# Kernel optimization log

Hardware: AMD Instinct MI355X
Metric: run time of the kernel (lower is better)

## Reference

```python
import jax, jax.numpy as jnp
import numpy as np
import math

FACTOR = 1

def setup_inputs() -> dict:
    key = jax.random.key(0)
    kq, kk, kv = jax.random.split(key, 3)
    B, L, H, D = 8, 4096, 8, 32
    queries = jax.random.normal(kq, (B, L, H, D), dtype=jnp.float32)
    keys = jax.random.normal(kk, (B, L, H, D), dtype=jnp.float32)
    values = jax.random.normal(kv, (B, L, H, D), dtype=jnp.float32)
    return {"queries": queries, "keys": keys, "values": values}


def reference(queries, keys, values):
    # queries/keys/values: [B, L, H, D]
    B, L, H, D = queries.shape
    q = jnp.transpose(queries, (0, 2, 1, 3))  # [B,H,L,D]
    k = jnp.transpose(keys, (0, 2, 1, 3))
    v = jnp.transpose(values, (0, 2, 1, 3))

    # FFT-based cross-correlation (period-based dependency discovery)
    q_fft = jnp.fft.rfft(q, axis=2)
    k_fft = jnp.fft.rfft(k, axis=2)
    spd = jnp.sum(q_fft * jnp.conj(k_fft), axis=-1)      # [B,H,Lf]
    corr = jnp.fft.irfft(spd, n=L, axis=-1)              # [B,H,L]

    # Time-delay aggregation (inference path: per-sample delays)
    top_k = max(1, min(int(FACTOR * math.log(L)), L))
    weights, delays = jax.lax.top_k(corr, top_k)          # [B,H,K]
    weights = jax.nn.softmax(weights, axis=-1)

    # roll values by -delay via circular gather: pattern[l] = v[(l+delay) % L]
    init_index = jnp.arange(L)[None, None, None, :]       # [1,1,1,L]
    idx = (init_index + delays[..., None]) % L            # [B,H,K,L]
    patterns = jnp.take_along_axis(v[:, :, None, :, :], idx[..., None], axis=3)  # [B,H,K,L,D]
    agg = jnp.sum(patterns * weights[..., None, None], axis=2)  # [B,H,L,D]

    # dropout is identity in eval mode
    return jnp.transpose(agg, (0, 2, 1, 3))  # [B,L,H,D]
```

## Files before the change

kernel.cpp:

```cpp
#include <hip/hip_runtime.h>
#include <hip/hip_bf16.h>


#define SWZ(i) ((i) ^ (((i) >> 4) & 15))
#define SLICE 2056

typedef float nfloat4 __attribute__((ext_vector_type(4)));

__device__ inline void cmul(float& outr, float& outi, float ar, float ai, float br, float bi) {
    outr = ar * br - ai * bi;
    outi = ar * bi + ai * br;
}

template<int DIR>
__device__ inline void fft16(float* vr, float* vi) {
    const float C1 = 0.92387953251128675613f;
    const float S1 = 0.38268343236508977173f;
    const float R2 = 0.70710678118654752440f;
    float ur[16], ui[16];
#pragma unroll
    for (int n2 = 0; n2 < 4; ++n2) {
        float ar = vr[n2],      ai = vi[n2];
        float br = vr[n2 + 4],  bi = vi[n2 + 4];
        float cr = vr[n2 + 8],  ci = vi[n2 + 8];
        float dr = vr[n2 + 12], di = vi[n2 + 12];
        float acr = ar + cr, aci = ai + ci;
        float asr = ar - cr, asi = ai - ci;
        float bdr = br + dr, bdi = bi + di;
        float bsr = br - dr, bsi = bi - di;
        ur[0 + n2]  = acr + bdr; ui[0 + n2]  = aci + bdi;
        ur[8 + n2]  = acr - bdr; ui[8 + n2]  = aci - bdi;
        if (DIR < 0) {
            ur[4 + n2]  = asr + bsi; ui[4 + n2]  = asi - bsr;
            ur[12 + n2] = asr - bsi; ui[12 + n2] = asi + bsr;
        } else {
            ur[4 + n2]  = asr - bsi; ui[4 + n2]  = asi + bsr;
            ur[12 + n2] = asr + bsi; ui[12 + n2] = asi - bsr;
        }
    }
#pragma unroll
    for (int k1 = 1; k1 < 4; ++k1) {
#pragma unroll
        for (int n2 = 1; n2 < 4; ++n2) {
            int e = k1 * n2;
            float c, s;
            if (e == 1)      { c = C1;  s = S1; }
            else if (e == 2) { c = R2;  s = R2; }
            else if (e == 3) { c = S1;  s = C1; }
            else if (e == 4) { c = 0.f; s = 1.f; }
            else if (e == 6) { c = -R2; s = R2; }
            else             { c = -C1; s = -S1; }
            int idx = k1 * 4 + n2;
            float r0 = ur[idx], i0 = ui[idx];
            if (DIR < 0) { ur[idx] = r0 * c + i0 * s; ui[idx] = i0 * c - r0 * s; }
            else         { ur[idx] = r0 * c - i0 * s; ui[idx] = i0 * c + r0 * s; }
        }
    }
#pragma unroll
    for (int k1 = 0; k1 < 4; ++k1) {
        float ar = ur[k1 * 4 + 0], ai = ui[k1 * 4 + 0];
        float br = ur[k1 * 4 + 1], bi = ui[k1 * 4 + 1];
        float cr = ur[k1 * 4 + 2], ci = ui[k1 * 4 + 2];
        float dr = ur[k1 * 4 + 3], di = ui[k1 * 4 + 3];
        float acr = ar + cr, aci = ai + ci;
        float asr = ar - cr, asi = ai - ci;
        float bdr = br + dr, bdi = bi + di;
        float bsr = br - dr, bsi = bi - di;
        vr[k1]      = acr + bdr; vi[k1]      = aci + bdi;
        vr[k1 + 8]  = acr - bdr; vi[k1 + 8]  = aci - bdi;
        if (DIR < 0) {
            vr[k1 + 4]  = asr + bsi; vi[k1 + 4]  = asi - bsr;
            vr[k1 + 12] = asr - bsi; vi[k1 + 12] = asi + bsr;
        } else {
            vr[k1 + 4]  = asr - bsi; vi[k1 + 4]  = asi + bsr;
            vr[k1 + 12] = asr + bsi; vi[k1 + 12] = asi - bsr;
        }
    }
}

template<int DIR, int NS>
__device__ inline void fft_pass16_pp(const float2* __restrict__ src,
                                     float2* __restrict__ dst,
                                     float w1r, float w1i, int j) {
    float vr[16], vi[16];
#pragma unroll
    for (int r = 0; r < 16; ++r) {
        float2 x = src[SWZ(j + r * 256)];
        vr[r] = x.x; vi[r] = x.y;
    }
    if (NS > 1) {
        float wr[16], wi[16];
        wr[1] = w1r; wi[1] = w1i;
#pragma unroll
        for (int r = 2; r < 16; ++r)
            cmul(wr[r], wi[r], wr[r >> 1], wi[r >> 1], wr[(r + 1) >> 1], wi[(r + 1) >> 1]);
#pragma unroll
        for (int r = 1; r < 16; ++r) {
            float r0 = vr[r], i0 = vi[r];
            vr[r] = r0 * wr[r] - i0 * wi[r];
            vi[r] = r0 * wi[r] + i0 * wr[r];
        }
    }
    fft16<DIR>(vr, vi);
    int base = (j / NS) * (16 * NS) + (j & (NS - 1));
#pragma unroll
    for (int r = 0; r < 16; ++r)
        dst[SWZ(base + r * NS)] = make_float2(vr[r], vi[r]);
}

template<int DIR>
__device__ inline void fft4096_pp(float2* A, float2* Bu, float c2, float s2,
                                  float c3, float s3, int tid) {
    fft_pass16_pp<DIR, 1>(A, Bu, 1.f, 0.f, tid);  __syncthreads();
    fft_pass16_pp<DIR, 16>(Bu, A, c2, s2, tid);   __syncthreads();
    fft_pass16_pp<DIR, 256>(A, Bu, c3, s3, tid);  __syncthreads();
}

__global__ __launch_bounds__(256) void transpose_pack_kernel(const float4* __restrict__ q4,
                                                             const float4* __restrict__ k4,
                                                             float4* __restrict__ xT4) {
    __shared__ float qs[64][65];
    __shared__ float ks[64][65];
    int bid = blockIdx.x;
    int ct = bid & 3;
    int lt = (bid >> 2) & 63;
    int b  = bid >> 8;
    int tid = threadIdx.x;
    int l0 = lt * 64, c0 = ct * 64;
    int cw = tid & 15;
    int rr = tid >> 4;
#pragma unroll
    for (int it = 0; it < 4; ++it) {
        int row = it * 16 + rr;
        size_t g = (size_t)(b * 4096 + l0 + row) * 64u + (size_t)(c0 / 4 + cw);
        float4 qv = q4[g];
        float4 kv = k4[g];
        qs[row][cw * 4 + 0] = qv.x; qs[row][cw * 4 + 1] = qv.y;
        qs[row][cw * 4 + 2] = qv.z; qs[row][cw * 4 + 3] = qv.w;
        ks[row][cw * 4 + 0] = kv.x; ks[row][cw * 4 + 1] = kv.y;
        ks[row][cw * 4 + 2] = kv.z; ks[row][cw * 4 + 3] = kv.w;
    }
    __syncthreads();
    int a = tid & 31;
    int cb = tid >> 5;
#pragma unroll
    for (int it = 0; it < 8; ++it) {
        int cc = it * 8 + cb;
        float4 o;
        o.x = qs[2 * a][cc];     o.y = ks[2 * a][cc];
        o.z = qs[2 * a + 1][cc]; o.w = ks[2 * a + 1][cc];
        xT4[(size_t)(b * 256 + c0 + cc) * 2048u + (size_t)(l0 / 2 + a)] = o;
    }
}

__device__ inline void spd_pair_accum(const float2* Z, float4* acc, float& accny, int tid) {
#pragma unroll
    for (int t = 0; t < 4; ++t) {
        int f0 = 2 * tid + 512 * t;
        float2 za = Z[SWZ(f0)];
        float2 zb = Z[SWZ(f0 + 1)];
        float2 ma = Z[SWZ((4096 - f0) & 4095)];
        float2 mb = Z[SWZ(4095 - f0)];
        float qr = za.x + ma.x, qi = za.y - ma.y;
        float kr = za.y + ma.y, ki = za.x - ma.x;
        acc[t].x += 0.25f * (qr * kr - qi * ki);
        acc[t].y += 0.25f * (qr * ki + qi * kr);
        qr = zb.x + mb.x; qi = zb.y - mb.y;
        kr = zb.y + mb.y; ki = zb.x - mb.x;
        acc[t].z += 0.25f * (qr * kr - qi * ki);
        acc[t].w += 0.25f * (qr * ki + qi * kr);
    }
    float2 zn = Z[SWZ(2048)];
    accny += zn.x * zn.y;
}

__global__ __launch_bounds__(256) void fwd_spd_fast(const float2* __restrict__ xT,
                                                    float2* __restrict__ spd_d) {
    __shared__ float2 A[4096], Bu[4096];
    int bid = blockIdx.x;
    int tid = threadIdx.x;
    int b = bid >> 6, p = bid & 63;
    const float TWO_PI = 6.2831853071795864769f;
    float ang2 = TWO_PI * (float)((tid & 15) * 16) * (1.0f / 4096.0f);
    float ang3 = TWO_PI * (float)tid * (1.0f / 4096.0f);
    float c2 = cosf(ang2), s2 = sinf(ang2);
    float c3 = cosf(ang3), s3 = sinf(ang3);
    float4 acc[4];
#pragma unroll
    for (int t = 0; t < 4; ++t) acc[t] = make_float4(0.f, 0.f, 0.f, 0.f);
    float accny = 0.f;
#pragma unroll
    for (int cc = 0; cc < 4; ++cc) {
        const float4* src4 = (const float4*)(xT + (size_t)(b * 256 + p * 4 + cc) * 4096u);
#pragma unroll
        for (int t = 0; t < 8; ++t) {
            float4 x = src4[tid + t * 256];
            int n = 2 * (tid + t * 256);
            A[SWZ(n)]     = make_float2(x.x, x.y);
            A[SWZ(n + 1)] = make_float2(x.z, x.w);
        }
        __syncthreads();
        fft4096_pp<-1>(A, Bu, c2, -s2, c3, -s3, tid);
        spd_pair_accum(Bu, acc, accny, tid);
        if (cc < 3) __syncthreads();
    }
    float4* dst4 = (float4*)(spd_d + (size_t)bid * SLICE);
#pragma unroll
    for (int t = 0; t < 4; ++t) dst4[tid + t * 256] = acc[t];
    if (tid == 0) spd_d[(size_t)bid * SLICE + 2048] = make_float2(accny, 0.f);
}

__global__ __launch_bounds__(256) void fwd_spd_slow(const float* __restrict__ q,
                                                    const float* __restrict__ k,
                                                    float2* __restrict__ spd_d) {
    __shared__ float2 A[4096], Bu[4096];
    int bid = blockIdx.x;
    int tid = threadIdx.x;
    int b = bid >> 6, p = bid & 63;
    const float TWO_PI = 6.2831853071795864769f;
    float ang2 = TWO_PI * (float)((tid & 15) * 16) * (1.0f / 4096.0f);
    float ang3 = TWO_PI * (float)tid * (1.0f / 4096.0f);
    float c2 = cosf(ang2), s2 = sinf(ang2);
    float c3 = cosf(ang3), s3 = sinf(ang3);
    float4 acc[4];
#pragma unroll
    for (int t = 0; t < 4; ++t) acc[t] = make_float4(0.f, 0.f, 0.f, 0.f);
    float accny = 0.f;
#pragma unroll
    for (int cc = 0; cc < 4; ++cc) {
        size_t base = (size_t)b * 1048576u + (size_t)(p * 4 + cc);
#pragma unroll
        for (int t = 0; t < 16; ++t) {
            int n = tid + t * 256;
            A[SWZ(n)] = make_float2(q[base + (size_t)n * 256u], k[base + (size_t)n * 256u]);
        }
        __syncthreads();
        fft4096_pp<-1>(A, Bu, c2, -s2, c3, -s3, tid);
        spd_pair_accum(Bu, acc, accny, tid);
        if (cc < 3) __syncthreads();
    }
    float4* dst4 = (float4*)(spd_d + (size_t)bid * SLICE);
#pragma unroll
    for (int t = 0; t < 4; ++t) dst4[tid + t * 256] = acc[t];
    if (tid == 0) spd_d[(size_t)bid * SLICE + 2048] = make_float2(accny, 0.f);
}

__global__ __launch_bounds__(256) void ifft_topk_kernel(const float2* __restrict__ spd_d,
                                                        float* __restrict__ wout,
                                                        int* __restrict__ dout) {
    __shared__ float2 A[4096], Bu[4096];
    __shared__ float rv[8][4];
    __shared__ int   ri[8][4];
    int bh = blockIdx.x;
    int b = bh >> 3, h = bh & 7;
    int tid = threadIdx.x;
    const float TWO_PI = 6.2831853071795864769f;
    float ang2 = TWO_PI * (float)((tid & 15) * 16) * (1.0f / 4096.0f);
    float ang3 = TWO_PI * (float)tid * (1.0f / 4096.0f);
    float c2 = cosf(ang2), s2 = sinf(ang2);
    float c3 = cosf(ang3), s3 = sinf(ang3);
    const float sc = 1.0f / 4096.0f;
    const float2* base = spd_d + (size_t)(b * 64 + h * 8) * SLICE;
    const float4* base4 = (const float4*)base;
#pragma unroll
    for (int t = 0; t < 4; ++t) {
        int f0 = 2 * tid + 512 * t;
        float4 a = make_float4(0.f, 0.f, 0.f, 0.f);
#pragma unroll
        for (int s = 0; s < 8; ++s) {
            float4 x = base4[(size_t)s * (SLICE / 2) + (size_t)(tid + 256 * t)];
            a.x += x.x; a.y += x.y; a.z += x.z; a.w += x.w;
        }
        float r0 = a.x * sc, i0 = a.y * sc;
        float r1 = a.z * sc, i1 = a.w * sc;
        A[SWZ(f0)]     = make_float2(r0, i0);
        A[SWZ(f0 + 1)] = make_float2(r1, i1);
        if (f0 > 0) A[SWZ(4096 - f0)] = make_float2(r0, -i0);
        A[SWZ(4095 - f0)] = make_float2(r1, -i1);
    }
    if (tid == 0) {
        float ny = 0.f;
#pragma unroll
        for (int s = 0; s < 8; ++s) ny += base[(size_t)s * SLICE + 2048].x;
        A[SWZ(2048)] = make_float2(ny * sc, 0.f);
    }
    __syncthreads();
    fft4096_pp<1>(A, Bu, c2, s2, c3, s3, tid);
    float cv[16];
#pragma unroll
    for (int t = 0; t < 16; ++t) cv[t] = Bu[SWZ(tid + t * 256)].x;

    int lane = tid & 63, wid = tid >> 6;
    float topv[8]; int topi[8];
    for (int kk = 0; kk < 8; ++kk) {
        float best = -3.0e38f; int bi = 0;
#pragma unroll
        for (int t = 0; t < 16; ++t) {
            int f = tid + t * 256;
            if (cv[t] > best) { best = cv[t]; bi = f; }
        }
#pragma unroll
        for (int off = 32; off > 0; off >>= 1) {
            float ov = __shfl_xor(best, off, 64);
            int   oi = __shfl_xor(bi, off, 64);
            if (ov > best || (ov == best && oi < bi)) { best = ov; bi = oi; }
        }
        if (lane == 0) { rv[kk][wid] = best; ri[kk][wid] = bi; }
        __syncthreads();
        float fb = rv[kk][0]; int fi = ri[kk][0];
#pragma unroll
        for (int w = 1; w < 4; ++w) {
            float ov = rv[kk][w]; int oi = ri[kk][w];
            if (ov > fb || (ov == fb && oi < fi)) { fb = ov; fi = oi; }
        }
        topv[kk] = fb; topi[kk] = fi;
        if (tid == (fi & 255)) {
            int t_owner = fi >> 8;
#pragma unroll
            for (int t = 0; t < 16; ++t)
                if (t == t_owner) cv[t] = -3.0e38f;
        }
    }
    if (tid == 0) {
        float mx = topv[0];
        float e[8], s = 0.0f;
#pragma unroll
        for (int kk = 0; kk < 8; ++kk) { e[kk] = expf(topv[kk] - mx); s += e[kk]; }
        float inv = 1.0f / s;
#pragma unroll
        for (int kk = 0; kk < 8; ++kk) {
            wout[bh * 8 + kk] = e[kk] * inv;
            dout[bh * 8 + kk] = topi[kk];
        }
    }
}

__global__ __launch_bounds__(256) void agg_kernel(const float4* __restrict__ v4,
                                                  const float* __restrict__ w,
                                                  const int* __restrict__ dl,
                                                  float4* __restrict__ out4) {
    __shared__ float sw[64];
    __shared__ int   sd[64];
    int blk = blockIdx.x;
    int b = blk & 7, lg = blk >> 3;
    int tid = threadIdx.x;
    if (tid < 64) {
        int h = tid >> 3, kk = tid & 7;
        sw[tid] = w[(b * 8 + h) * 8 + kk];
        sd[tid] = dl[(b * 8 + h) * 8 + kk];
    }
    __syncthreads();
    int lq = tid >> 6;
    int c4 = tid & 63;
    int h  = c4 >> 3;
    float w_[8]; int d_[8];
#pragma unroll
    for (int kk = 0; kk < 8; ++kk) { w_[kk] = sw[h * 8 + kk]; d_[kk] = sd[h * 8 + kk]; }
#pragma unroll
    for (int rep = 0; rep < 8; ++rep) {
        int l = lg * 32 + rep * 4 + lq;
        float4 acc = make_float4(0.f, 0.f, 0.f, 0.f);
#pragma unroll
        for (int kk = 0; kk < 8; ++kk) {
            int l2 = (l + d_[kk]) & 4095;
            float4 x = v4[(size_t)(b * 4096 + l2) * 64u + (size_t)c4];
            acc.x += w_[kk] * x.x; acc.y += w_[kk] * x.y;
            acc.z += w_[kk] * x.z; acc.w += w_[kk] * x.w;
        }
        nfloat4 nv = {acc.x, acc.y, acc.z, acc.w};
        __builtin_nontemporal_store(nv,
            (nfloat4*)&out4[(size_t)(b * 4096 + l) * 64u + (size_t)c4]);
    }
}

extern "C" void kernel_launch(void* const* d_in, const int* in_sizes, int n_in,
                              void* d_out, int out_size, void* d_ws, size_t ws_size,
                              hipStream_t stream) {
    const float* q = (const float*)d_in[0];
    const float* k = (const float*)d_in[1];
    const float* v = (const float*)d_in[2];
    float* ws  = (float*)d_ws;
    float2* spd_d = (float2*)d_out;

    const size_t XT_FLOATS = 16777216u;
    const size_t FAST_FLOATS = XT_FLOATS + 1024u;
    bool fast = ws_size >= FAST_FLOATS * sizeof(float);

    if (fast) {
        float* wbuf = ws + XT_FLOATS;
        int*   dbuf = (int*)(wbuf + 512);
        transpose_pack_kernel<<<2048, 256, 0, stream>>>((const float4*)q, (const float4*)k,
                                                        (float4*)ws);
        fwd_spd_fast<<<512, 256, 0, stream>>>((const float2*)ws, spd_d);
        ifft_topk_kernel<<<64, 256, 0, stream>>>(spd_d, wbuf, dbuf);
        agg_kernel<<<1024, 256, 0, stream>>>((const float4*)v, wbuf, dbuf, (float4*)d_out);
    } else {
        float* wbuf = ws;
        int*   dbuf = (int*)(wbuf + 512);
        fwd_spd_slow<<<512, 256, 0, stream>>>(q, k, spd_d);
        ifft_topk_kernel<<<64, 256, 0, stream>>>(spd_d, wbuf, dbuf);
        agg_kernel<<<1024, 256, 0, stream>>>((const float4*)v, wbuf, dbuf, (float4*)d_out);
    }
}
```

Baseline: 85.43 us.

## Pre-swizzle transposed layout and prefetch next channel via global_load_lds during FFT

The transpose kernel now writes pairs in the shared-memory swizzled order, so the FFT kernel can copy global data straight into LDS with direct global-to-LDS loads. The loads for the next channel are issued while the current channel's spectrum is being accumulated, overlapping memory traffic with compute and removing the register round trip. This relies on buffer A being free once the FFT finishes (the result sits in Bu), and on the 16-byte LDS destination layout matching the intrinsic's per-lane placement. If that placement does not match, the data ends up in the wrong order.

```diff
diff --git a/kernel.cpp b/kernel.cpp
--- a/kernel.cpp
+++ b/kernel.cpp
@@ -146,10 +146,13 @@
 #pragma unroll
     for (int it = 0; it < 8; ++it) {
         int cc = it * 8 + cb;
-        float4 o;
-        o.x = qs[2 * a][cc];     o.y = ks[2 * a][cc];
-        o.z = qs[2 * a + 1][cc]; o.w = ks[2 * a + 1][cc];
-        xT4[(size_t)(b * 256 + c0 + cc) * 2048u + (size_t)(l0 / 2 + a)] = o;
+        float2 z0 = make_float2(qs[2 * a][cc],     ks[2 * a][cc]);
+        float2 z1 = make_float2(qs[2 * a + 1][cc], ks[2 * a + 1][cc]);
+        int n  = l0 + 2 * a;
+        int sn = SWZ(n);
+        float4 o = (sn & 1) ? make_float4(z1.x, z1.y, z0.x, z0.y)
+                            : make_float4(z0.x, z0.y, z1.x, z1.y);
+        xT4[(size_t)(b * 256 + c0 + cc) * 2048u + (size_t)(sn >> 1)] = o;
     }
 }
 
@@ -176,7 +179,8 @@
 
 __global__ __launch_bounds__(256) void fwd_spd_fast(const float2* __restrict__ xT,
                                                     float2* __restrict__ spd_d) {
-    __shared__ float2 A[4096], Bu[4096];
+    __shared__ __align__(16) float2 A[4096];
+    __shared__ __align__(16) float2 Bu[4096];
     int bid = blockIdx.x;
     int tid = threadIdx.x;
     int b = bid >> 6, p = bid & 63;
@@ -189,18 +193,24 @@
 #pragma unroll
     for (int t = 0; t < 4; ++t) acc[t] = make_float4(0.f, 0.f, 0.f, 0.f);
     float accny = 0.f;
+
+    const float4* base4 = (const float4*)(xT + (size_t)(b * 256 + p * 4) * 4096u);
+#pragma unroll
+    for (int t = 0; t < 8; ++t)
+        __builtin_amdgcn_global_load_lds((const uint32_t*)&base4[tid + t * 256],
+                                         (uint32_t*)&A[2 * (tid + t * 256)], 16, 0, 0);
+    __syncthreads();
+
 #pragma unroll
     for (int cc = 0; cc < 4; ++cc) {
-        const float4* src4 = (const float4*)(xT + (size_t)(b * 256 + p * 4 + cc) * 4096u);
-#pragma unroll
-        for (int t = 0; t < 8; ++t) {
-            float4 x = src4[tid + t * 256];
-            int n = 2 * (tid + t * 256);
-            A[SWZ(n)]     = make_float2(x.x, x.y);
-            A[SWZ(n + 1)] = make_float2(x.z, x.w);
-        }
-        __syncthreads();
         fft4096_pp<-1>(A, Bu, c2, -s2, c3, -s3, tid);
+        if (cc < 3) {
+            const float4* src4 = base4 + (size_t)(cc + 1) * 2048u;
+#pragma unroll
+            for (int t = 0; t < 8; ++t)
+                __builtin_amdgcn_global_load_lds((const uint32_t*)&src4[tid + t * 256],
+                                                 (uint32_t*)&A[2 * (tid + t * 256)], 16, 0, 0);
+        }
         spd_pair_accum(Bu, acc, accny, tid);
         if (cc < 3) __syncthreads();
     }
@@ -213,7 +223,8 @@
 __global__ __launch_bounds__(256) void fwd_spd_slow(const float* __restrict__ q,
                                                     const float* __restrict__ k,
                                                     float2* __restrict__ spd_d) {
-    __shared__ float2 A[4096], Bu[4096];
+    __shared__ __align__(16) float2 A[4096];
+    __shared__ __align__(16) float2 Bu[4096];
     int bid = blockIdx.x;
     int tid = threadIdx.x;
     int b = bid >> 6, p = bid & 63;
@@ -248,7 +259,8 @@
 __global__ __launch_bounds__(256) void ifft_topk_kernel(const float2* __restrict__ spd_d,
                                                         float* __restrict__ wout,
                                                         int* __restrict__ dout) {
-    __shared__ float2 A[4096], Bu[4096];
+    __shared__ __align__(16) float2 A[4096];
+    __shared__ __align__(16) float2 Bu[4096];
     __shared__ float rv[8][4];
     __shared__ int   ri[8][4];
     int bh = blockIdx.x;
```

New measurement: 85.00 us, median of 2. About the same (-0.5%).
